# Kernel tuning notes

Hardware: AMD Instinct MI355X
Metric: run time of the kernel (lower is better)

Reference implementation:

```python
import jax, jax.numpy as jnp
import numpy as np

N_E = 100000       # entities
N_R = 1000         # relations
N_CLASSES = 20000  # class_index.max() + 1
E = 1000000        # edges (triples)
E_HIDDEN = 256
C_HIDDEN = 128
R_HIDDEN = 128
NEG_SLOPE = 0.01   # F.leaky_relu default


def leaky_relu(x):
    return jnp.where(x >= 0, x, NEG_SLOPE * x)


def segment_softmax(x, idx, num_segments):
    # torch_geometric-style scatter softmax over segments given by idx
    m = jax.ops.segment_max(x, idx, num_segments=num_segments)
    ex = jnp.exp(x - m[idx])
    s = jax.ops.segment_sum(ex, idx, num_segments=num_segments)
    return ex / (s[idx] + 1e-16)


def setup_inputs() -> dict:
    key = jax.random.key(0)
    ks = jax.random.split(key, 20)
    inv_c = 1.0 / np.sqrt(C_HIDDEN)
    inv_r = 1.0 / np.sqrt(R_HIDDEN)
    inv_e = 1.0 / np.sqrt(E_HIDDEN)
    inp = {
        "x_e": jax.random.normal(ks[0], (N_E, E_HIDDEN), jnp.float32),
        "edge_index": jax.random.randint(ks[1], (2, E), 0, N_E),
        "rel": jax.random.randint(ks[2], (E,), 0, N_R),
        "triple_num": jax.random.randint(ks[3], (E,), 0, N_E),
        "r_emb": jax.random.normal(ks[4], (N_R, R_HIDDEN), jnp.float32),
        "class_index": jax.random.randint(ks[5], (E,), 0, N_CLASSES),
        "head_class": jax.random.randint(ks[6], (N_CLASSES,), 0, N_E),
        # attention projection vectors (Linear(c_hidden,1,bias=False) weights)
        "a_h1": jax.random.normal(ks[7], (C_HIDDEN,), jnp.float32) * inv_c,
        "a_h2": jax.random.normal(ks[8], (C_HIDDEN,), jnp.float32) * inv_c,
        "a_h3": jax.random.normal(ks[9], (C_HIDDEN,), jnp.float32) * inv_c,
        "a_h4": jax.random.normal(ks[10], (C_HIDDEN,), jnp.float32) * inv_c,
        "a_t1": jax.random.normal(ks[11], (C_HIDDEN,), jnp.float32) * inv_c,
        "a_t2": jax.random.normal(ks[12], (C_HIDDEN,), jnp.float32) * inv_c,
        "a_t3": jax.random.normal(ks[13], (C_HIDDEN,), jnp.float32) * inv_c,
        "a_r1": jax.random.normal(ks[14], (R_HIDDEN,), jnp.float32) * inv_r,
        "a_r2": jax.random.normal(ks[15], (R_HIDDEN,), jnp.float32) * inv_r,
        "a_c": jax.random.normal(ks[16], (C_HIDDEN,), jnp.float32) * inv_c,
        # entity->class-space projections [e_hidden, c_hidden]
        "w_h": jax.random.normal(ks[17], (E_HIDDEN, C_HIDDEN), jnp.float32) * inv_e,
        "w_t": jax.random.normal(ks[18], (E_HIDDEN, C_HIDDEN), jnp.float32) * inv_e,
        # highway gate Linear(c_hidden, c_hidden)
        "hw_w": jax.random.normal(ks[19], (C_HIDDEN, C_HIDDEN), jnp.float32) * inv_c,
        "hw_b": jnp.zeros((C_HIDDEN,), jnp.float32),
    }
    return inp


def reference(x_e, edge_index, rel, triple_num, r_emb, class_index, head_class,
              a_h1, a_h2, a_h3, a_h4, a_t1, a_t2, a_t3, a_r1, a_r2, a_c,
              w_h, w_t, hw_w, hw_b):
    h_idx = edge_index[0]
    t_idx = edge_index[1]

    x_r_h = jax.nn.relu(x_e @ w_h)   # [N_e, C]
    x_r_t = jax.nn.relu(x_e @ w_t)   # [N_e, C]

    # --- level 1: edge attention over triple_num segments ---
    e1 = ((x_r_h @ a_h1)[h_idx] + (x_r_t @ a_t1)[t_idx]) / 2 + (r_emb @ a_r1)[rel]
    alpha = segment_softmax(leaky_relu(e1), triple_num, N_E)       # [E]

    x_t = x_r_t[t_idx] * alpha[:, None]                            # [E, C]
    norm = jnp.linalg.norm(x_t, axis=1, keepdims=True)
    x_t = x_t / jnp.maximum(norm, 1e-12)                           # F.normalize p=2

    # --- level 2: relation/class attention over class_index segments ---
    e_t = x_t @ a_t2                                               # [E]
    e_h = (x_r_h @ a_h2)[h_idx]
    e_r = (r_emb @ a_r2)[rel]
    e_r = (e_r + ((x_r_h @ a_h3)[h_idx] + (x_t @ a_t3)) / 2) / 2
    beta = segment_softmax(leaky_relu(e_t + e_r + e_h), class_index, N_CLASSES)

    # spmm: A[class_index[i], t_idx[i]] = beta[i];  x_class = A @ x_t
    x_class = jax.ops.segment_sum(beta[:, None] * x_t[t_idx],
                                  class_index, num_segments=N_CLASSES)  # [N_CLASSES, C]

    # --- level 3: class->head-entity attention over head_class segments ---
    e_c = (x_class @ a_c) + (x_r_h @ a_h4)[head_class]             # [N_CLASSES]
    gama = segment_softmax(leaky_relu(e_c), head_class, N_E)
    x_e_h = jax.ops.segment_sum(gama[:, None] * x_class,
                                head_class, num_segments=N_E)      # [N_e, C]

    # highway combine
    gate = jax.nn.sigmoid(x_r_h @ hw_w + hw_b)
    return gate * x_e_h + (1.0 - gate) * x_r_h
```

## Files before the change

### kernel.cpp

```cpp
#include <hip/hip_runtime.h>
#include <hip/hip_bf16.h>

#define LRELU(x) ((x) >= 0.f ? (x) : 0.01f * (x))

typedef __attribute__((ext_vector_type(8))) short short8v;
typedef __attribute__((ext_vector_type(4))) float f32x4;

__device__ inline unsigned fenc(float x) {
    unsigned u = __float_as_uint(x);
    return (u & 0x80000000u) ? ~u : (u | 0x80000000u);
}
__device__ inline float fdec(unsigned e) {
    return __uint_as_float((e & 0x80000000u) ? (e ^ 0x80000000u) : ~e);
}

__device__ inline float wred(float v) {
#pragma unroll
    for (int o = 32; o > 0; o >>= 1) v += __shfl_xor(v, o, 64);
    return v;
}
__device__ inline float wredmax(float v) {
#pragma unroll
    for (int o = 32; o > 0; o >>= 1) v = fmaxf(v, __shfl_xor(v, o, 64));
    return v;
}

__device__ inline unsigned short f2bu(float x) {
    __hip_bfloat16 b = __float2bfloat16(x);
    return *reinterpret_cast<unsigned short*>(&b);
}
__device__ inline float bu2f(unsigned short u) {
    return __uint_as_float((unsigned)u << 16);
}

__device__ inline f32x4 mfma16(short8v a, short8v b, f32x4 c) {
    return __builtin_amdgcn_mfma_f32_16x16x32_bf16(a, b, c, 0, 0, 0);
}

__device__ inline void gload16(const void* g, void* l) {
    __builtin_amdgcn_global_load_lds(
        (const __attribute__((address_space(1))) void*)g,
        (__attribute__((address_space(3))) void*)l, 16, 0, 0);
}

__global__ __launch_bounds__(256) void k_convW(
    const float* __restrict__ wh, const float* __restrict__ wt,
    const float* __restrict__ hww, unsigned short* __restrict__ wtb_hi,
    unsigned short* __restrict__ hwt_hi) {
    int id = blockIdx.x * 256 + threadIdx.x;
    if (id < 256 * 256) {
        int n = id >> 8, k = id & 255;
        float v = (n < 128) ? wh[(size_t)k * 128 + n] : wt[(size_t)k * 128 + (n - 128)];
        wtb_hi[(size_t)n * 256 + k] = f2bu(v);
    } else {
        int id2 = id - 256 * 256;
        if (id2 < 128 * 128) {
            int n = id2 >> 7, k = id2 & 127;
            hwt_hi[(size_t)n * 128 + k] = f2bu(hww[(size_t)k * 128 + n]);
        }
    }
}

__global__ __launch_bounds__(256) void k_rel(const float* __restrict__ remb,
                                             const float* __restrict__ ar2,
                                             float* __restrict__ er2, int NR) {
    int lane = threadIdx.x & 63;
    int r = blockIdx.x * 4 + (threadIdx.x >> 6);
    if (r >= NR) return;
    float v0 = remb[(size_t)r * 128 + lane];
    float v1 = remb[(size_t)r * 128 + 64 + lane];
    float p2 = wred(v0 * ar2[lane] + v1 * ar2[64 + lane]);
    if (lane == 0) er2[r] = p2;
}

template <int EPI>
__device__ __forceinline__ void mm_body(
    const float* __restrict__ Af32, const unsigned short* __restrict__ Ah,
    const unsigned short* __restrict__ Bh,
    unsigned short* __restrict__ oh0, unsigned short* __restrict__ oh1,
    float* __restrict__ o0, const float* __restrict__ bias,
    const float* __restrict__ xeh, const unsigned* __restrict__ m3f, int M,
    const float* __restrict__ ah2, const float* __restrict__ ah3,
    const float* __restrict__ ah4, const float* __restrict__ at2,
    const float* __restrict__ at3,
    float* __restrict__ hb, float* __restrict__ eh4o,
    float2* __restrict__ pta, const int* __restrict__ tidxg) {
    constexpr int KD = (EPI == 0) ? 256 : 128;
    constexpr int NSTEP = KD / 32;
    __shared__ float As_f[(EPI == 0) ? 2 : 1][(EPI == 0) ? 128 * 32 : 16];
    __shared__ unsigned short As_h[(EPI == 1) ? 2 : 1][(EPI == 1) ? 128 * 32 : 16];
    __shared__ unsigned short Bs_h[2][128 * 32];

    int bx = blockIdx.x;
    int half = (EPI == 0) ? (bx & 1) : 0;
    int mblk = (EPI == 0) ? (bx >> 1) : bx;
    int row0 = mblk * 128;
    if (row0 + 128 > M) row0 = M - 128;
    int tid = threadIdx.x, w = tid >> 6, l = tid & 63;
    int lr = l & 15, hi4 = l >> 4;
    int srow = l >> 2, sslot = l & 3;
    int arow = l >> 3, afi = l & 7;

    f32x4 acc[2][8];
#pragma unroll
    for (int i = 0; i < 2; i++)
#pragma unroll
        for (int j = 0; j < 8; j++) acc[i][j] = (f32x4){0.f, 0.f, 0.f, 0.f};

    auto stage = [&](int s, int b) {
        int k0 = s * 32;
        constexpr int NU = (EPI == 0) ? 6 : 4;
#pragma unroll
        for (int i = 0; i < NU; i++) {
            int u = w * NU + i;
            if constexpr (EPI == 0) {
                if (u < 16) {
                    int row = u * 8 + arow;
                    int sf = ((afi ^ arow) << 2);
                    gload16(Af32 + (size_t)(row0 + row) * KD + k0 + sf,
                            (char*)&As_f[b][0] + u * 1024);
                } else {
                    int ub = u - 16;
                    int row = ub * 16 + srow;
                    int klog = (sslot ^ ((row >> 1) & 3)) * 8;
                    gload16(Bh + (size_t)(half * 128 + row) * KD + k0 + klog,
                            (char*)&Bs_h[b][0] + ub * 1024);
                }
            } else {
                int arr = u >> 3, ld = u & 7;
                int row = ld * 16 + srow;
                int klog = (sslot ^ ((row >> 1) & 3)) * 8;
                if (arr == 0)
                    gload16(Ah + (size_t)(row0 + row) * KD + k0 + klog,
                            (char*)&As_h[b][0] + ld * 1024);
                else
                    gload16(Bh + (size_t)row * KD + k0 + klog,
                            (char*)&Bs_h[b][0] + ld * 1024);
            }
        }
    };

    stage(0, 0);
    __syncthreads();
    for (int s = 0; s < NSTEP; s++) {
        int b = s & 1;
        if (s + 1 < NSTEP) stage(s + 1, b ^ 1);

        short8v am_h[2];
#pragma unroll
        for (int mr = 0; mr < 2; mr++) {
            int r = w * 32 + mr * 16 + lr;
            if constexpr (EPI == 0) {
                int s0 = ((2 * hi4 + 0) ^ (r & 7)) * 4;
                int s1 = ((2 * hi4 + 1) ^ (r & 7)) * 4;
                float4 f0 = *(const float4*)&As_f[b][r * 32 + s0];
                float4 f1 = *(const float4*)&As_f[b][r * 32 + s1];
                short8v v;
                v[0] = (short)f2bu(f0.x); v[1] = (short)f2bu(f0.y);
                v[2] = (short)f2bu(f0.z); v[3] = (short)f2bu(f0.w);
                v[4] = (short)f2bu(f1.x); v[5] = (short)f2bu(f1.y);
                v[6] = (short)f2bu(f1.z); v[7] = (short)f2bu(f1.w);
                am_h[mr] = v;
            } else {
                int ko = (hi4 ^ ((r >> 1) & 3)) * 8;
                am_h[mr] = *(const short8v*)&As_h[b][r * 32 + ko];
            }
        }
#pragma unroll
        for (int ncc = 0; ncc < 8; ncc += 4) {
            short8v bn_h[4];
#pragma unroll
            for (int j = 0; j < 4; j++) {
                int n = (ncc + j) * 16 + lr;
                int ko = (hi4 ^ ((n >> 1) & 3)) * 8;
                bn_h[j] = *(const short8v*)&Bs_h[b][n * 32 + ko];
            }
#pragma unroll
            for (int mr = 0; mr < 2; mr++)
#pragma unroll
                for (int j = 0; j < 4; j++)
                    acc[mr][ncc + j] = mfma16(am_h[mr], bn_h[j], acc[mr][ncc + j]);
        }
        __syncthreads();
    }

    if constexpr (EPI == 0) {
        unsigned short* OH = half ? oh1 : oh0;
        const float* v1 = half ? at2 : ah2;
        const float* v2 = half ? at3 : ah3;
#pragma unroll
        for (int mr = 0; mr < 2; mr++)
#pragma unroll
            for (int rr = 0; rr < 4; rr++) {
                int row = row0 + w * 32 + mr * 16 + hi4 * 4 + rr;
                float d0 = 0.f, d1 = 0.f, d2 = 0.f;
#pragma unroll
                for (int nc = 0; nc < 8; nc++) {
                    float v = fmaxf(acc[mr][nc][rr], 0.f);
                    int col = nc * 16 + lr;
                    d0 = fmaf(v, v1[col], d0);
                    d1 = fmaf(v, v2[col], d1);
                    d2 = half ? fmaf(v, v, d2) : fmaf(v, ah4[col], d2);
                }
#pragma unroll
                for (int o = 1; o <= 8; o <<= 1) {
                    d0 += __shfl_xor(d0, o, 64);
                    d1 += __shfl_xor(d1, o, 64);
                    d2 += __shfl_xor(d2, o, 64);
                }
                float inv = 1.f;
                if (half) inv = 1.f / fmaxf(sqrtf(d2), 1e-12f);
#pragma unroll
                for (int nc = 0; nc < 8; nc++) {
                    float v = fmaxf(acc[mr][nc][rr], 0.f);
                    OH[(size_t)row * 128 + nc * 16 + lr] = f2bu(half ? v * inv : v);
                }
                if (lr == 0) {
                    if (half == 0) {
                        hb[row] = d0 + 0.25f * d1;
                        eh4o[row] = d2;
                    } else {
                        float tav = (d0 + 0.25f * d1) * inv;
                        pta[row] = make_float2(tav, __int_as_float(tidxg[row]));
                    }
                }
            }
    } else {
#pragma unroll
        for (int mr = 0; mr < 2; mr++)
#pragma unroll
            for (int rr = 0; rr < 4; rr++) {
                int row = row0 + w * 32 + mr * 16 + hi4 * 4 + rr;
                bool touched = (m3f[row] != 0u);
#pragma unroll
                for (int nc = 0; nc < 8; nc++) {
                    int col = nc * 16 + lr;
                    float a = acc[mr][nc][rr] + bias[col];
                    float g = 1.f / (1.f + expf(-a));
                    size_t o = (size_t)row * 128 + col;
                    float af = bu2f(Ah[o]);
                    float xv = 0.f;
                    if (touched) xv = xeh[o];
                    o0[o] = g * xv + (1.f - g) * af;
                }
            }
    }
}

__global__ __launch_bounds__(256) void k_mm_proj(
    const float* Af32, const unsigned short* Bh,
    unsigned short* oh0, unsigned short* oh1, int M,
    const float* ah2, const float* ah3, const float* ah4,
    const float* at2, const float* at3,
    float* hb, float* eh4o, float2* pta, const int* tidxg) {
    mm_body<0>(Af32, nullptr, Bh, oh0, oh1, nullptr, nullptr, nullptr, nullptr,
               M, ah2, ah3, ah4, at2, at3, hb, eh4o, pta, tidxg);
}

__global__ __launch_bounds__(256) void k_mm_hw(
    const unsigned short* Ah, const unsigned short* Bh,
    float* o0, const float* bias, const float* xeh, const unsigned* m3f, int M) {
    mm_body<1>(nullptr, Ah, Bh, nullptr, nullptr, o0, bias, xeh, m3f, M,
               nullptr, nullptr, nullptr, nullptr, nullptr,
               nullptr, nullptr, nullptr, nullptr);
}

__global__ __launch_bounds__(256) void k_hist(const int* __restrict__ cidx,
                                              int* __restrict__ cnt, int E) {
    int i = blockIdx.x * 256 + threadIdx.x;
    if (i >= E) return;
    atomicAdd(&cnt[cidx[i]], 1);
}

__global__ __launch_bounds__(1024) void k_scan(const int* __restrict__ cnt,
                                               int* __restrict__ off,
                                               int* __restrict__ cur, int NC) {
    __shared__ int wt[16];
    __shared__ int sbase;
    int tid = threadIdx.x, w = tid >> 6, lane = tid & 63;
    if (tid == 0) sbase = 0;
    __syncthreads();
    for (int c0 = 0; c0 < NC; c0 += 1024) {
        int c = c0 + tid;
        int v = (c < NC) ? cnt[c] : 0;
        int x = v;
#pragma unroll
        for (int o = 1; o < 64; o <<= 1) {
            int t = __shfl_up(x, o, 64);
            if (lane >= o) x += t;
        }
        if (lane == 63) wt[w] = x;
        __syncthreads();
        int pre = 0, tot = 0;
#pragma unroll
        for (int i = 0; i < 16; i++) {
            int t = wt[i];
            tot += t;
            if (i < w) pre += t;
        }
        int excl = sbase + pre + x - v;
        if (c < NC) { off[c] = excl; cur[c] = excl; }
        __syncthreads();
        if (tid == 0) sbase += tot;
        __syncthreads();
    }
}

__global__ __launch_bounds__(256) void k_edgescatter(
    const int* __restrict__ cidx, int* __restrict__ cur,
    const int* __restrict__ hidx, const int* __restrict__ tidx,
    const int* __restrict__ rel, const float2* __restrict__ pta,
    const float* __restrict__ hb, const float* __restrict__ er2,
    float2* __restrict__ e2gs, int E) {
    int i = blockIdx.x * 256 + threadIdx.x;
    if (i >= E) return;
    int pos = atomicAdd(&cur[cidx[i]], 1);
    float2 p = pta[tidx[i]];
    float z2 = p.x + hb[hidx[i]] + 0.5f * er2[rel[i]];
    e2gs[pos] = make_float2(LRELU(z2), p.y);
}

__global__ __launch_bounds__(256) void k_spmm2(
    const int* __restrict__ off, const int* __restrict__ cnt,
    const float2* __restrict__ e2gs, const unsigned* __restrict__ xrtn_b,
    float* __restrict__ xclass, const float* __restrict__ ac,
    const float* __restrict__ eh4, const int* __restrict__ hclass,
    float* __restrict__ zc, unsigned* __restrict__ m3, int NC) {
    int lane = threadIdx.x & 63;
    int c = blockIdx.x * 4 + (threadIdx.x >> 6);
    if (c >= NC) return;
    int n = cnt[c];
    float a0 = 0.f, a1 = 0.f;
    if (n > 0) {
        int base = off[c];
        float m = -3.4e38f, s = 0.f;
        for (int j = lane; j < n; j += 64) {
            float z = e2gs[base + j].x;
            if (z > m) { s = s * __expf(m - z) + 1.f; m = z; }
            else s += __expf(z - m);
        }
        float M = wredmax(m);
        s = wred(s * __expf(m - M));
        float inv = 1.f / (s + 1e-16f);
        for (int j0 = 0; j0 < n; j0 += 64) {
            int lim = n - j0;
            if (lim > 64) lim = 64;
            float wv = 0.f;
            int g = 0;
            if (lane < lim) {
                float2 pg = e2gs[base + j0 + lane];
                wv = __expf(pg.x - M) * inv;
                g = __float_as_int(pg.y);
            }
            int jj = 0;
            for (; jj + 8 <= lim; jj += 8) {
                float w0 = __shfl(wv, jj + 0), w1 = __shfl(wv, jj + 1);
                float w2 = __shfl(wv, jj + 2), w3 = __shfl(wv, jj + 3);
                float w4 = __shfl(wv, jj + 4), w5 = __shfl(wv, jj + 5);
                float w6 = __shfl(wv, jj + 6), w7 = __shfl(wv, jj + 7);
                unsigned u0 = xrtn_b[(size_t)__shfl(g, jj + 0) * 64 + lane];
                unsigned u1 = xrtn_b[(size_t)__shfl(g, jj + 1) * 64 + lane];
                unsigned u2 = xrtn_b[(size_t)__shfl(g, jj + 2) * 64 + lane];
                unsigned u3 = xrtn_b[(size_t)__shfl(g, jj + 3) * 64 + lane];
                unsigned u4 = xrtn_b[(size_t)__shfl(g, jj + 4) * 64 + lane];
                unsigned u5 = xrtn_b[(size_t)__shfl(g, jj + 5) * 64 + lane];
                unsigned u6 = xrtn_b[(size_t)__shfl(g, jj + 6) * 64 + lane];
                unsigned u7 = xrtn_b[(size_t)__shfl(g, jj + 7) * 64 + lane];
                a0 = fmaf(w0, bu2f((unsigned short)(u0 & 0xffff)), a0);
                a1 = fmaf(w0, bu2f((unsigned short)(u0 >> 16)), a1);
                a0 = fmaf(w1, bu2f((unsigned short)(u1 & 0xffff)), a0);
                a1 = fmaf(w1, bu2f((unsigned short)(u1 >> 16)), a1);
                a0 = fmaf(w2, bu2f((unsigned short)(u2 & 0xffff)), a0);
                a1 = fmaf(w2, bu2f((unsigned short)(u2 >> 16)), a1);
                a0 = fmaf(w3, bu2f((unsigned short)(u3 & 0xffff)), a0);
                a1 = fmaf(w3, bu2f((unsigned short)(u3 >> 16)), a1);
                a0 = fmaf(w4, bu2f((unsigned short)(u4 & 0xffff)), a0);
                a1 = fmaf(w4, bu2f((unsigned short)(u4 >> 16)), a1);
                a0 = fmaf(w5, bu2f((unsigned short)(u5 & 0xffff)), a0);
                a1 = fmaf(w5, bu2f((unsigned short)(u5 >> 16)), a1);
                a0 = fmaf(w6, bu2f((unsigned short)(u6 & 0xffff)), a0);
                a1 = fmaf(w6, bu2f((unsigned short)(u6 >> 16)), a1);
                a0 = fmaf(w7, bu2f((unsigned short)(u7 & 0xffff)), a0);
                a1 = fmaf(w7, bu2f((unsigned short)(u7 >> 16)), a1);
            }
            for (; jj < lim; jj++) {
                float wj = __shfl(wv, jj);
                unsigned u = xrtn_b[(size_t)__shfl(g, jj) * 64 + lane];
                a0 = fmaf(wj, bu2f((unsigned short)(u & 0xffff)), a0);
                a1 = fmaf(wj, bu2f((unsigned short)(u >> 16)), a1);
            }
        }
    }
    *(float2*)&xclass[(size_t)c * 128 + 2 * lane] = make_float2(a0, a1);
    float p = wred(a0 * ac[2 * lane] + a1 * ac[2 * lane + 1]);
    if (lane == 0) {
        int hc = hclass[c];
        float z = LRELU(p + eh4[hc]);
        zc[c] = z;
        atomicMax(&m3[hc], fenc(z));
    }
}

__global__ __launch_bounds__(256) void k_class2(
    const int* __restrict__ hclass, float* __restrict__ zc,
    const unsigned* __restrict__ m3, float* __restrict__ s3,
    float* __restrict__ xeh, int NC) {
    int lane = threadIdx.x & 63;
    int c = blockIdx.x * 4 + (threadIdx.x >> 6);
    if (c >= NC) return;
    int hc = hclass[c];
    *(float2*)&xeh[(size_t)hc * 128 + 2 * lane] = make_float2(0.f, 0.f);
    if (lane == 0) {
        float ex = expf(zc[c] - fdec(m3[hc]));
        zc[c] = ex;
        atomicAdd(&s3[hc], ex);
    }
}

__global__ __launch_bounds__(256) void k_class3(
    const int* __restrict__ hclass, const float* __restrict__ zc,
    const float* __restrict__ s3, const float* __restrict__ xclass,
    float* __restrict__ xeh, int NC) {
    int lane = threadIdx.x & 63;
    int c = blockIdx.x * 4 + (threadIdx.x >> 6);
    if (c >= NC) return;
    int hc = hclass[c];
    float gama = zc[c] / (s3[hc] + 1e-16f);
    float v0 = xclass[(size_t)c * 128 + lane], v1 = xclass[(size_t)c * 128 + 64 + lane];
    atomicAdd(&xeh[(size_t)hc * 128 + lane], gama * v0);
    atomicAdd(&xeh[(size_t)hc * 128 + 64 + lane], gama * v1);
}

extern "C" void kernel_launch(void* const* d_in, const int* in_sizes, int n_in,
                              void* d_out, int out_size, void* d_ws, size_t ws_size,
                              hipStream_t stream) {
    (void)n_in; (void)out_size; (void)ws_size;
    const float* xe   = (const float*)d_in[0];
    const int*   eidx = (const int*)d_in[1];
    const int*   rel  = (const int*)d_in[2];
    const float* remb = (const float*)d_in[4];
    const int*   cidx = (const int*)d_in[5];
    const int*   hcls = (const int*)d_in[6];
    const float* ah2  = (const float*)d_in[8];
    const float* ah3  = (const float*)d_in[9];
    const float* ah4  = (const float*)d_in[10];
    const float* at2  = (const float*)d_in[12];
    const float* at3  = (const float*)d_in[13];
    const float* ar2  = (const float*)d_in[15];
    const float* ac   = (const float*)d_in[16];
    const float* wh   = (const float*)d_in[17];
    const float* wt   = (const float*)d_in[18];
    const float* hww  = (const float*)d_in[19];
    const float* hwb  = (const float*)d_in[20];
    float* out = (float*)d_out;

    const int NE = in_sizes[0] / 256;
    const int E  = in_sizes[2];
    const int NR = in_sizes[4] / 128;
    const int NC = in_sizes[6];
    const int* hidx = eidx;
    const int* tidx = eidx + E;

    char* base = (char*)d_ws;
    size_t off0 = 0;
    auto alloc = [&](size_t bytes) -> char* {
        char* r = base + off0;
        off0 = (off0 + bytes + 255) & ~(size_t)255;
        return r;
    };
    float* hb   = (float*)alloc((size_t)NE * 4);
    float* eh4b = (float*)alloc((size_t)NE * 4);
    float2* pta = (float2*)alloc((size_t)NE * 8);
    float* er2b = (float*)alloc((size_t)NR * 4);
    float2* e2gs = (float2*)alloc((size_t)E * 8);
    float* zc   = (float*)alloc((size_t)NC * 4);
    unsigned short* wtb_hi = (unsigned short*)alloc((size_t)256 * 256 * 2);
    unsigned short* hwt_hi = (unsigned short*)alloc((size_t)128 * 128 * 2);
    unsigned short* xrh_hi = (unsigned short*)alloc((size_t)NE * 128 * 2);
    unsigned short* xrtn   = (unsigned short*)alloc((size_t)NE * 128 * 2);
    int* offb = (int*)alloc((size_t)NC * 4);
    int* curb = (int*)alloc((size_t)NC * 4);
    float* xclass = (float*)alloc((size_t)NC * 128 * 4);
    float* xeh    = (float*)alloc((size_t)NE * 128 * 4);
    size_t zoff = off0;
    unsigned* m3 = (unsigned*)alloc((size_t)NE * 4);
    float* s3    = (float*)alloc((size_t)NE * 4);
    int* cntb    = (int*)alloc((size_t)NC * 4);
    size_t zbytes = off0 - zoff;

    hipMemsetAsync(base + zoff, 0, zbytes, stream);

    k_convW<<<(256 * 256 + 128 * 128 + 255) / 256, 256, 0, stream>>>(
        wh, wt, hww, wtb_hi, hwt_hi);
    k_rel<<<(NR + 3) / 4, 256, 0, stream>>>(remb, ar2, er2b, NR);

    k_mm_proj<<<((NE + 127) / 128) * 2, 256, 0, stream>>>(
        xe, wtb_hi, xrh_hi, xrtn, NE,
        ah2, ah3, ah4, at2, at3, hb, eh4b, pta, tidx);

    k_hist<<<(E + 255) / 256, 256, 0, stream>>>(cidx, cntb, E);
    k_scan<<<1, 1024, 0, stream>>>(cntb, offb, curb, NC);

    k_edgescatter<<<(E + 255) / 256, 256, 0, stream>>>(
        cidx, curb, hidx, tidx, rel, pta, hb, er2b, e2gs, E);

    k_spmm2<<<(NC + 3) / 4, 256, 0, stream>>>(offb, cntb, e2gs,
                                              (const unsigned*)xrtn, xclass,
                                              ac, eh4b, hcls, zc, m3, NC);
    k_class2<<<(NC + 3) / 4, 256, 0, stream>>>(hcls, zc, m3, s3, xeh, NC);
    k_class3<<<(NC + 3) / 4, 256, 0, stream>>>(hcls, zc, s3, xclass, xeh, NC);

    k_mm_hw<<<(NE + 127) / 128, 256, 0, stream>>>(
        xrh_hi, hwt_hi, out, hwb, xeh, m3, NE);
}
```

Before: 282.3 us.

## Compute both projection halves in one 512-thread block to share A tile loads

The projection GEMM previously launched two blocks per 128-row tile, one per output half (w_h and w_t), each loading the same fp32 x_e tile. Now a single 512-thread block loads the A tile once and computes both 128-column halves, with waves 0-3 handling the head projection and waves 4-7 the tail. This halves global reads of the 256-wide fp32 input and the fp32-to-bf16 conversion work, at the cost of double the LDS for B and fewer, larger blocks. The hw GEMM is split out into its own kernel without functional change.

```diff
diff --git a/kernel.cpp b/kernel.cpp
--- a/kernel.cpp
+++ b/kernel.cpp
@@ -73,30 +73,23 @@
     if (lane == 0) er2[r] = p2;
 }
 
-template <int EPI>
-__device__ __forceinline__ void mm_body(
-    const float* __restrict__ Af32, const unsigned short* __restrict__ Ah,
-    const unsigned short* __restrict__ Bh,
-    unsigned short* __restrict__ oh0, unsigned short* __restrict__ oh1,
-    float* __restrict__ o0, const float* __restrict__ bias,
-    const float* __restrict__ xeh, const unsigned* __restrict__ m3f, int M,
+__global__ __launch_bounds__(512) void k_mm_proj(
+    const float* __restrict__ Af32, const unsigned short* __restrict__ Bh,
+    unsigned short* __restrict__ oh0, unsigned short* __restrict__ oh1, int M,
     const float* __restrict__ ah2, const float* __restrict__ ah3,
     const float* __restrict__ ah4, const float* __restrict__ at2,
     const float* __restrict__ at3,
     float* __restrict__ hb, float* __restrict__ eh4o,
     float2* __restrict__ pta, const int* __restrict__ tidxg) {
-    constexpr int KD = (EPI == 0) ? 256 : 128;
+    constexpr int KD = 256;
     constexpr int NSTEP = KD / 32;
-    __shared__ float As_f[(EPI == 0) ? 2 : 1][(EPI == 0) ? 128 * 32 : 16];
-    __shared__ unsigned short As_h[(EPI == 1) ? 2 : 1][(EPI == 1) ? 128 * 32 : 16];
-    __shared__ unsigned short Bs_h[2][128 * 32];
-
-    int bx = blockIdx.x;
-    int half = (EPI == 0) ? (bx & 1) : 0;
-    int mblk = (EPI == 0) ? (bx >> 1) : bx;
-    int row0 = mblk * 128;
+    __shared__ float As_f[2][128 * 32];
+    __shared__ unsigned short Bs_h[2][256 * 32];
+
+    int row0 = blockIdx.x * 128;
     if (row0 + 128 > M) row0 = M - 128;
     int tid = threadIdx.x, w = tid >> 6, l = tid & 63;
+    int rg = w & 3, ch = w >> 2;
     int lr = l & 15, hi4 = l >> 4;
     int srow = l >> 2, sslot = l & 3;
     int arow = l >> 3, afi = l & 7;
@@ -109,33 +102,20 @@
 
     auto stage = [&](int s, int b) {
         int k0 = s * 32;
-        constexpr int NU = (EPI == 0) ? 6 : 4;
-#pragma unroll
-        for (int i = 0; i < NU; i++) {
-            int u = w * NU + i;
-            if constexpr (EPI == 0) {
-                if (u < 16) {
-                    int row = u * 8 + arow;
-                    int sf = ((afi ^ arow) << 2);
-                    gload16(Af32 + (size_t)(row0 + row) * KD + k0 + sf,
-                            (char*)&As_f[b][0] + u * 1024);
-                } else {
-                    int ub = u - 16;
-                    int row = ub * 16 + srow;
-                    int klog = (sslot ^ ((row >> 1) & 3)) * 8;
-                    gload16(Bh + (size_t)(half * 128 + row) * KD + k0 + klog,
-                            (char*)&Bs_h[b][0] + ub * 1024);
-                }
+#pragma unroll
+        for (int i = 0; i < 4; i++) {
+            int u = w * 4 + i;
+            if (u < 16) {
+                int row = u * 8 + arow;
+                int sf = ((afi ^ arow) << 2);
+                gload16(Af32 + (size_t)(row0 + row) * KD + k0 + sf,
+                        (char*)&As_f[b][0] + u * 1024);
             } else {
-                int arr = u >> 3, ld = u & 7;
-                int row = ld * 16 + srow;
-                int klog = (sslot ^ ((row >> 1) & 3)) * 8;
-                if (arr == 0)
-                    gload16(Ah + (size_t)(row0 + row) * KD + k0 + klog,
-                            (char*)&As_h[b][0] + ld * 1024);
-                else
-                    gload16(Bh + (size_t)row * KD + k0 + klog,
-                            (char*)&Bs_h[b][0] + ld * 1024);
+                int ub = u - 16;
+                int n = ub * 16 + srow;
+                int klog = (sslot ^ ((n >> 1) & 3)) * 8;
+                gload16(Bh + (size_t)n * KD + k0 + klog,
+                        (char*)&Bs_h[b][0] + ub * 1024);
             }
         }
     };
@@ -149,22 +129,127 @@
         short8v am_h[2];
 #pragma unroll
         for (int mr = 0; mr < 2; mr++) {
+            int r = rg * 32 + mr * 16 + lr;
+            int s0 = ((2 * hi4 + 0) ^ (r & 7)) * 4;
+            int s1 = ((2 * hi4 + 1) ^ (r & 7)) * 4;
+            float4 f0 = *(const float4*)&As_f[b][r * 32 + s0];
+            float4 f1 = *(const float4*)&As_f[b][r * 32 + s1];
+            short8v v;
+            v[0] = (short)f2bu(f0.x); v[1] = (short)f2bu(f0.y);
+            v[2] = (short)f2bu(f0.z); v[3] = (short)f2bu(f0.w);
+            v[4] = (short)f2bu(f1.x); v[5] = (short)f2bu(f1.y);
+            v[6] = (short)f2bu(f1.z); v[7] = (short)f2bu(f1.w);
+            am_h[mr] = v;
+        }
+#pragma unroll
+        for (int ncc = 0; ncc < 8; ncc += 4) {
+            short8v bn_h[4];
+#pragma unroll
+            for (int j = 0; j < 4; j++) {
+                int n = ch * 128 + (ncc + j) * 16 + lr;
+                int ko = (hi4 ^ ((n >> 1) & 3)) * 8;
+                bn_h[j] = *(const short8v*)&Bs_h[b][n * 32 + ko];
+            }
+#pragma unroll
+            for (int mr = 0; mr < 2; mr++)
+#pragma unroll
+                for (int j = 0; j < 4; j++)
+                    acc[mr][ncc + j] = mfma16(am_h[mr], bn_h[j], acc[mr][ncc + j]);
+        }
+        __syncthreads();
+    }
+
+    unsigned short* OH = ch ? oh1 : oh0;
+    const float* v1 = ch ? at2 : ah2;
+    const float* v2 = ch ? at3 : ah3;
+#pragma unroll
+    for (int mr = 0; mr < 2; mr++)
+#pragma unroll
+        for (int rr = 0; rr < 4; rr++) {
+            int row = row0 + rg * 32 + mr * 16 + hi4 * 4 + rr;
+            float d0 = 0.f, d1 = 0.f, d2 = 0.f;
+#pragma unroll
+            for (int nc = 0; nc < 8; nc++) {
+                float v = fmaxf(acc[mr][nc][rr], 0.f);
+                int col = nc * 16 + lr;
+                d0 = fmaf(v, v1[col], d0);
+                d1 = fmaf(v, v2[col], d1);
+                d2 = ch ? fmaf(v, v, d2) : fmaf(v, ah4[col], d2);
+            }
+#pragma unroll
+            for (int o = 1; o <= 8; o <<= 1) {
+                d0 += __shfl_xor(d0, o, 64);
+                d1 += __shfl_xor(d1, o, 64);
+                d2 += __shfl_xor(d2, o, 64);
+            }
+            float inv = 1.f;
+            if (ch) inv = 1.f / fmaxf(sqrtf(d2), 1e-12f);
+#pragma unroll
+            for (int nc = 0; nc < 8; nc++) {
+                float v = fmaxf(acc[mr][nc][rr], 0.f);
+                OH[(size_t)row * 128 + nc * 16 + lr] = f2bu(ch ? v * inv : v);
+            }
+            if (lr == 0) {
+                if (ch == 0) {
+                    hb[row] = d0 + 0.25f * d1;
+                    eh4o[row] = d2;
+                } else {
+                    float tav = (d0 + 0.25f * d1) * inv;
+                    pta[row] = make_float2(tav, __int_as_float(tidxg[row]));
+                }
+            }
+        }
+}
+
+__global__ __launch_bounds__(256) void k_mm_hw(
+    const unsigned short* __restrict__ Ah, const unsigned short* __restrict__ Bh,
+    float* __restrict__ o0, const float* __restrict__ bias,
+    const float* __restrict__ xeh, const unsigned* __restrict__ m3f, int M) {
+    constexpr int KD = 128;
+    constexpr int NSTEP = KD / 32;
+    __shared__ unsigned short As_h[2][128 * 32];
+    __shared__ unsigned short Bs_h[2][128 * 32];
+
+    int row0 = blockIdx.x * 128;
+    if (row0 + 128 > M) row0 = M - 128;
+    int tid = threadIdx.x, w = tid >> 6, l = tid & 63;
+    int lr = l & 15, hi4 = l >> 4;
+    int srow = l >> 2, sslot = l & 3;
+
+    f32x4 acc[2][8];
+#pragma unroll
+    for (int i = 0; i < 2; i++)
+#pragma unroll
+        for (int j = 0; j < 8; j++) acc[i][j] = (f32x4){0.f, 0.f, 0.f, 0.f};
+
+    auto stage = [&](int s, int b) {
+        int k0 = s * 32;
+#pragma unroll
+        for (int i = 0; i < 4; i++) {
+            int u = w * 4 + i;
+            int arr = u >> 3, ld = u & 7;
+            int row = ld * 16 + srow;
+            int klog = (sslot ^ ((row >> 1) & 3)) * 8;
+            if (arr == 0)
+                gload16(Ah + (size_t)(row0 + row) * KD + k0 + klog,
+                        (char*)&As_h[b][0] + ld * 1024);
+            else
+                gload16(Bh + (size_t)row * KD + k0 + klog,
+                        (char*)&Bs_h[b][0] + ld * 1024);
+        }
+    };
+
+    stage(0, 0);
+    __syncthreads();
+    for (int s = 0; s < NSTEP; s++) {
+        int b = s & 1;
+        if (s + 1 < NSTEP) stage(s + 1, b ^ 1);
+        short8v am_h[2];
+#pragma unroll
+        for (int mr = 0; mr < 2; mr++) {
             int r = w * 32 + mr * 16 + lr;
-            if constexpr (EPI == 0) {
-                int s0 = ((2 * hi4 + 0) ^ (r & 7)) * 4;
-                int s1 = ((2 * hi4 + 1) ^ (r & 7)) * 4;
-                float4 f0 = *(const float4*)&As_f[b][r * 32 + s0];
-                float4 f1 = *(const float4*)&As_f[b][r * 32 + s1];
-                short8v v;
-                v[0] = (short)f2bu(f0.x); v[1] = (short)f2bu(f0.y);
-                v[2] = (short)f2bu(f0.z); v[3] = (short)f2bu(f0.w);
-                v[4] = (short)f2bu(f1.x); v[5] = (short)f2bu(f1.y);
-                v[6] = (short)f2bu(f1.z); v[7] = (short)f2bu(f1.w);
-                am_h[mr] = v;
-            } else {
-                int ko = (hi4 ^ ((r >> 1) & 3)) * 8;
-                am_h[mr] = *(const short8v*)&As_h[b][r * 32 + ko];
-            }
+            int ko = (hi4 ^ ((r >> 1) & 3)) * 8;
+            am_h[mr] = *(const short8v*)&As_h[b][r * 32 + ko];
         }
 #pragma unroll
         for (int ncc = 0; ncc < 8; ncc += 4) {
@@ -184,85 +269,24 @@
         __syncthreads();
     }
 
-    if constexpr (EPI == 0) {
-        unsigned short* OH = half ? oh1 : oh0;
-        const float* v1 = half ? at2 : ah2;
-        const float* v2 = half ? at3 : ah3;
-#pragma unroll
-        for (int mr = 0; mr < 2; mr++)
-#pragma unroll
-            for (int rr = 0; rr < 4; rr++) {
-                int row = row0 + w * 32 + mr * 16 + hi4 * 4 + rr;
-                float d0 = 0.f, d1 = 0.f, d2 = 0.f;
-#pragma unroll
-                for (int nc = 0; nc < 8; nc++) {
-                    float v = fmaxf(acc[mr][nc][rr], 0.f);
-                    int col = nc * 16 + lr;
-                    d0 = fmaf(v, v1[col], d0);
-                    d1 = fmaf(v, v2[col], d1);
-                    d2 = half ? fmaf(v, v, d2) : fmaf(v, ah4[col], d2);
-                }
-#pragma unroll
-                for (int o = 1; o <= 8; o <<= 1) {
-                    d0 += __shfl_xor(d0, o, 64);
-                    d1 += __shfl_xor(d1, o, 64);
-                    d2 += __shfl_xor(d2, o, 64);
-                }
-                float inv = 1.f;
-                if (half) inv = 1.f / fmaxf(sqrtf(d2), 1e-12f);
-#pragma unroll
-                for (int nc = 0; nc < 8; nc++) {
-                    float v = fmaxf(acc[mr][nc][rr], 0.f);
-                    OH[(size_t)row * 128 + nc * 16 + lr] = f2bu(half ? v * inv : v);
-                }
-                if (lr == 0) {
-                    if (half == 0) {
-                        hb[row] = d0 + 0.25f * d1;
-                        eh4o[row] = d2;
-                    } else {
-                        float tav = (d0 + 0.25f * d1) * inv;
-                        pta[row] = make_float2(tav, __int_as_float(tidxg[row]));
-                    }
-                }
-            }
-    } else {
-#pragma unroll
-        for (int mr = 0; mr < 2; mr++)
-#pragma unroll
-            for (int rr = 0; rr < 4; rr++) {
-                int row = row0 + w * 32 + mr * 16 + hi4 * 4 + rr;
-                bool touched = (m3f[row] != 0u);
-#pragma unroll
-                for (int nc = 0; nc < 8; nc++) {
-                    int col = nc * 16 + lr;
-                    float a = acc[mr][nc][rr] + bias[col];
-                    float g = 1.f / (1.f + expf(-a));
-                    size_t o = (size_t)row * 128 + col;
-                    float af = bu2f(Ah[o]);
-                    float xv = 0.f;
-                    if (touched) xv = xeh[o];
-                    o0[o] = g * xv + (1.f - g) * af;
-                }
-            }
-    }
-}
-
-__global__ __launch_bounds__(256) void k_mm_proj(
-    const float* Af32, const unsigned short* Bh,
-    unsigned short* oh0, unsigned short* oh1, int M,
-    const float* ah2, const float* ah3, const float* ah4,
-    const float* at2, const float* at3,
-    float* hb, float* eh4o, float2* pta, const int* tidxg) {
-    mm_body<0>(Af32, nullptr, Bh, oh0, oh1, nullptr, nullptr, nullptr, nullptr,
-               M, ah2, ah3, ah4, at2, at3, hb, eh4o, pta, tidxg);
-}
-
-__global__ __launch_bounds__(256) void k_mm_hw(
-    const unsigned short* Ah, const unsigned short* Bh,
-    float* o0, const float* bias, const float* xeh, const unsigned* m3f, int M) {
-    mm_body<1>(nullptr, Ah, Bh, nullptr, nullptr, o0, bias, xeh, m3f, M,
-               nullptr, nullptr, nullptr, nullptr, nullptr,
-               nullptr, nullptr, nullptr, nullptr);
+#pragma unroll
+    for (int mr = 0; mr < 2; mr++)
+#pragma unroll
+        for (int rr = 0; rr < 4; rr++) {
+            int row = row0 + w * 32 + mr * 16 + hi4 * 4 + rr;
+            bool touched = (m3f[row] != 0u);
+#pragma unroll
+            for (int nc = 0; nc < 8; nc++) {
+                int col = nc * 16 + lr;
+                float a = acc[mr][nc][rr] + bias[col];
+                float g = 1.f / (1.f + expf(-a));
+                size_t o = (size_t)row * 128 + col;
+                float af = bu2f(Ah[o]);
+                float xv = 0.f;
+                if (touched) xv = xeh[o];
+                o0[o] = g * xv + (1.f - g) * af;
+            }
+        }
 }
 
 __global__ __launch_bounds__(256) void k_hist(const int* __restrict__ cidx,
@@ -494,7 +518,7 @@
         wh, wt, hww, wtb_hi, hwt_hi);
     k_rel<<<(NR + 3) / 4, 256, 0, stream>>>(remb, ar2, er2b, NR);
 
-    k_mm_proj<<<((NE + 127) / 128) * 2, 256, 0, stream>>>(
+    k_mm_proj<<<(NE + 127) / 128, 512, 0, stream>>>(
         xe, wtb_hi, xrh_hi, xrtn, NE,
         ah2, ah3, ah4, at2, at3, hb, eh4b, pta, tidx);
 
```

Result: faster. 276.1 us (-2.2%).
